# Kernel tuning notes

Hardware: AMD Instinct MI355X
Metric: run time of the kernel (lower is better)

## Reference

```python
import jax, jax.numpy as jnp
import numpy as np

N_NODES = 100000
N_EDGES = 1600000
IN_FEATS = 256
OUT_FEATS = 128


def setup_inputs() -> dict:
    key = jax.random.key(0)
    k1, k2, k3, k4, k5 = jax.random.split(key, 5)
    x = jax.random.normal(k1, (N_NODES, IN_FEATS), dtype=jnp.float32)
    edge_row = jax.random.randint(k2, (N_EDGES,), 0, N_NODES, dtype=jnp.int64 if jax.config.jax_enable_x64 else jnp.int32)
    edge_col = jax.random.randint(k3, (N_EDGES,), 0, N_NODES, dtype=jnp.int64 if jax.config.jax_enable_x64 else jnp.int32)
    edge_val = jax.random.uniform(k4, (N_EDGES,), dtype=jnp.float32)
    # xavier_uniform-like init for weight
    limit = float(np.sqrt(6.0 / (IN_FEATS + OUT_FEATS)))
    weight = jax.random.uniform(k5, (IN_FEATS, OUT_FEATS), dtype=jnp.float32, minval=-limit, maxval=limit)
    b = jnp.zeros((OUT_FEATS,), dtype=jnp.float32)
    return {"x": x, "edge_row": edge_row, "edge_col": edge_col, "edge_val": edge_val, "weight": weight, "b": b}


def reference(x, edge_row, edge_col, edge_val, weight, b):
    # sup = input @ weight : [N, out_feats]
    sup = x @ weight
    # out = spmm(adj, sup): gather source rows, scale by edge value, scatter-add to dest
    msgs = edge_val[:, None] * sup[edge_col]          # [E, out_feats]
    out = jax.ops.segment_sum(msgs, edge_row, num_segments=N_NODES)  # [N, out_feats]
    return out + b
```

## Files before the change

### kernel.cpp

```cpp
#include <hip/hip_runtime.h>


#define K_FEATS 256
#define N_FEATS 128
#define BSHIFT 7
#define BROWS 128
#define BCAP 3072
#define STASH 12
#define CHUNK 8192
#define EPT 32
#define RMOD 5

typedef __attribute__((ext_vector_type(8))) short short8;
typedef __attribute__((ext_vector_type(4))) float float4v;

__device__ __forceinline__ unsigned short f2bf(float f) {
    unsigned int u = __float_as_uint(f);
    unsigned int r = u + 0x7FFF + ((u >> 16) & 1);
    return (unsigned short)(r >> 16);
}

__global__ __launch_bounds__(256) void prep_w(const float* __restrict__ w,
                                              unsigned short* __restrict__ wt) {
    int n = blockIdx.x;
    int k = threadIdx.x;
    wt[n * K_FEATS + k] = f2bf(w[k * N_FEATS + n]);
}

__global__ __launch_bounds__(256) void zero_ints(int* __restrict__ p, int n) {
    int i = blockIdx.x * 256 + threadIdx.x;
    if (i < n) p[i] = 0;
}

__global__ __launch_bounds__(256) void gemm_partition(
        const float* __restrict__ x, const unsigned short* __restrict__ wt,
        unsigned short* __restrict__ sup, int M, int NT,
        const int* __restrict__ erow, const int* __restrict__ ecol,
        const float* __restrict__ eval_, int* __restrict__ bcur,
        int2* __restrict__ tmp, int E, int NB, int NCH) {
    __shared__ int hist[1024];
    __shared__ int cur[1024];
    const int g   = blockIdx.x;
    const int tid = threadIdx.x;

    if (g % RMOD == 0) {
        int pid = g / RMOD;
        if (pid >= NCH) return;
        const long e0 = (long)pid * CHUNK;

        for (int i = tid; i < NB; i += 256) hist[i] = 0;
        __syncthreads();

        int rows[EPT];
#pragma unroll
        for (int i = 0; i < EPT; i++) {
            long e = e0 + tid + i * 256;
            int r = -1;
            if (e < E) {
                r = erow[e];
                atomicAdd(&hist[r >> BSHIFT], 1);
            }
            rows[i] = r;
        }
        __syncthreads();

        for (int i = tid; i < NB; i += 256) {
            int c = hist[i];
            cur[i] = c ? atomicAdd(&bcur[i], c) : 0;
        }
        __syncthreads();

#pragma unroll
        for (int i = 0; i < EPT; i++) {
            long e = e0 + tid + i * 256;
            if (e >= E) continue;
            int r = rows[i];
            int b = r >> BSHIFT;
            int p = atomicAdd(&cur[b], 1);
            if (p < BCAP)
                tmp[(long)b * BCAP + p] = make_int2(((r & (BROWS - 1)) << 17) | ecol[e],
                                                    __float_as_int(eval_[e]));
        }
        return;
    }

    int tile = g - g / RMOD - 1;
    if (tile >= NT) return;

    const int wv   = tid >> 6;
    const int lane = tid & 63;
    const int l15  = lane & 15;
    const int quad = lane >> 4;
    const int row0 = tile * 128 + wv * 32;

    float4v acc[2][8];
#pragma unroll
    for (int mt = 0; mt < 2; mt++)
#pragma unroll
        for (int nt = 0; nt < 8; nt++) acc[mt][nt] = (float4v)(0.f);

#pragma unroll 2
    for (int k0 = 0; k0 < K_FEATS; k0 += 32) {
        short8 afrag[2];
#pragma unroll
        for (int mt = 0; mt < 2; mt++) {
            int grow = row0 + mt * 16 + l15;
            float4 a0 = make_float4(0.f, 0.f, 0.f, 0.f);
            float4 a1 = make_float4(0.f, 0.f, 0.f, 0.f);
            if (grow < M) {
                const float* p = x + (long)grow * K_FEATS + k0 + quad * 8;
                a0 = *(const float4*)p;
                a1 = *(const float4*)(p + 4);
            }
            short8 af;
            af[0] = (short)f2bf(a0.x); af[1] = (short)f2bf(a0.y);
            af[2] = (short)f2bf(a0.z); af[3] = (short)f2bf(a0.w);
            af[4] = (short)f2bf(a1.x); af[5] = (short)f2bf(a1.y);
            af[6] = (short)f2bf(a1.z); af[7] = (short)f2bf(a1.w);
            afrag[mt] = af;
        }
        short8 bfrag[8];
#pragma unroll
        for (int nt = 0; nt < 8; nt++) {
            bfrag[nt] = *(const short8*)(wt + (nt * 16 + l15) * K_FEATS + k0 + quad * 8);
        }
#pragma unroll
        for (int mt = 0; mt < 2; mt++)
#pragma unroll
            for (int nt = 0; nt < 8; nt++)
                acc[mt][nt] = __builtin_amdgcn_mfma_f32_16x16x32_bf16(
                    afrag[mt], bfrag[nt], acc[mt][nt], 0, 0, 0);
    }

#pragma unroll
    for (int mt = 0; mt < 2; mt++) {
#pragma unroll
        for (int reg = 0; reg < 4; reg++) {
            int grow = row0 + mt * 16 + quad * 4 + reg;
            if (grow < M) {
#pragma unroll
                for (int nt = 0; nt < 8; nt++) {
                    sup[(long)grow * N_FEATS + nt * 16 + l15] = f2bf(acc[mt][nt][reg]);
                }
            }
        }
    }
}

__global__ __launch_bounds__(256) void bucket_spmm(const int* __restrict__ bcnt,
                                                   const int2* __restrict__ tmp,
                                                   const unsigned short* __restrict__ sup,
                                                   const float* __restrict__ b,
                                                   float* __restrict__ out, int M) {
    __shared__ int hist[BROWS];
    __shared__ int rs[BROWS];
    __shared__ int cur[BROWS];
    __shared__ __align__(16) int2 se[BCAP];
    const int bkt  = blockIdx.x;
    const int tid  = threadIdx.x;
    const int wv   = tid >> 6;
    const int lane = tid & 63;
    const int row0 = bkt << BSHIFT;

    if (tid < BROWS) hist[tid] = 0;
    __syncthreads();

    int cnt = bcnt[bkt];
    if (cnt > BCAP) cnt = BCAP;
    const int2* t = tmp + (long)bkt * BCAP;

    int2 stash[STASH];
#pragma unroll
    for (int j = 0; j < STASH; j++) {
        int i = tid + j * 256;
        if (i < cnt) {
            int2 e = t[i];
            stash[j] = e;
            atomicAdd(&hist[(unsigned)e.x >> 17], 1);
        }
    }
    __syncthreads();

    if (tid < BROWS) cur[tid] = hist[tid];
    __syncthreads();
#pragma unroll
    for (int s = 1; s < BROWS; s <<= 1) {
        int v = 0;
        if (tid >= s && tid < BROWS) v = cur[tid - s];
        __syncthreads();
        if (tid < BROWS) cur[tid] += v;
        __syncthreads();
    }
    if (tid < BROWS) {
        int start = cur[tid] - hist[tid];
        rs[tid]  = start;
        cur[tid] = start;
    }
    __syncthreads();

#pragma unroll
    for (int j = 0; j < STASH; j++) {
        int i = tid + j * 256;
        if (i < cnt) {
            int2 e = stash[j];
            int rl = (unsigned)e.x >> 17;
            int p = atomicAdd(&cur[rl], 1);
            se[p] = make_int2(e.x & 0x1FFFF, e.y);
        }
    }
    __syncthreads();

    const int half = lane >> 5;
    const int l31  = lane & 31;
    const uint2* sup64 = (const uint2*)sup;
    const float4v bb = ((const float4v*)b)[l31];

    for (int rr = 0; rr < 32; rr++) {
        int r    = wv * 32 + rr;
        int grow = row0 + r;
        if (grow >= M) break;
        int s  = rs[r];
        int e2 = s + hist[r];

        float4v acc = (float4v)(0.f);
        int base = s;
        for (; base + 8 <= e2; base += 8) {
            int2 ed[4];
#pragma unroll
            for (int u = 0; u < 4; u++) ed[u] = se[base + half + 2 * u];
            uint2 g[4];
#pragma unroll
            for (int u = 0; u < 4; u++) g[u] = sup64[(long)ed[u].x * 32 + l31];
#pragma unroll
            for (int u = 0; u < 4; u++) {
                float v = __int_as_float(ed[u].y);
                acc.x += v * __uint_as_float(g[u].x << 16);
                acc.y += v * __uint_as_float(g[u].x & 0xFFFF0000u);
                acc.z += v * __uint_as_float(g[u].y << 16);
                acc.w += v * __uint_as_float(g[u].y & 0xFFFF0000u);
            }
        }
        for (int i = base + half; i < e2; i += 2) {
            int2 ed = se[i];
            uint2 g = sup64[(long)ed.x * 32 + l31];
            float v = __int_as_float(ed.y);
            acc.x += v * __uint_as_float(g.x << 16);
            acc.y += v * __uint_as_float(g.x & 0xFFFF0000u);
            acc.z += v * __uint_as_float(g.y << 16);
            acc.w += v * __uint_as_float(g.y & 0xFFFF0000u);
        }

        acc.x += __shfl_xor(acc.x, 32);
        acc.y += __shfl_xor(acc.y, 32);
        acc.z += __shfl_xor(acc.z, 32);
        acc.w += __shfl_xor(acc.w, 32);

        if (half == 0) {
            float4v o = acc + bb;
            *(float4v*)(out + (long)grow * N_FEATS + l31 * 4) = o;
        }
    }
}

extern "C" void kernel_launch(void* const* d_in, const int* in_sizes, int n_in,
                              void* d_out, int out_size, void* d_ws, size_t ws_size,
                              hipStream_t stream) {
    const float* x     = (const float*)d_in[0];
    const int*   erow  = (const int*)d_in[1];
    const int*   ecol  = (const int*)d_in[2];
    const float* eval_ = (const float*)d_in[3];
    const float* w     = (const float*)d_in[4];
    const float* b     = (const float*)d_in[5];
    float* out = (float*)d_out;

    const int M   = in_sizes[0] / K_FEATS;
    const int E   = in_sizes[1];
    const int NB  = (M + BROWS - 1) >> BSHIFT;
    const int NT  = (M + 127) / 128;
    const int NCH = (E + CHUNK - 1) / CHUNK;

    size_t o_sup  = 0;
    size_t o_wt   = o_sup  + (((size_t)M * N_FEATS * 2 + 15) & ~15ul);
    size_t o_bcur = o_wt   + (size_t)K_FEATS * N_FEATS * 2;
    size_t o_tmp  = o_bcur + (((size_t)NB * 4 + 15) & ~15ul);

    unsigned short* sup  = (unsigned short*)((char*)d_ws + o_sup);
    unsigned short* wt   = (unsigned short*)((char*)d_ws + o_wt);
    int*            bcur = (int*)((char*)d_ws + o_bcur);
    int2*           tmp  = (int2*)((char*)d_ws + o_tmp);

    prep_w<<<N_FEATS, 256, 0, stream>>>(w, wt);
    zero_ints<<<(NB + 255) / 256, 256, 0, stream>>>(bcur, NB);

    gemm_partition<<<NT + NCH, 256, 0, stream>>>(x, wt, sup, M, NT,
                                                 erow, ecol, eval_, bcur, tmp, E, NB, NCH);

    bucket_spmm<<<NB, 256, 0, stream>>>(bcur, tmp, sup, b, out, M);
}
```

Baseline: 317.5 us.

## Split GEMM into bf16 conversion pass and LDS-staged MFMA GEMM; widen SpMM blocks

The fused partition kernel now only converts x to bf16 into a workspace buffer alongside the edge bucketing. A separate GEMM kernel streams the bf16 tiles into swizzled LDS with global_load_lds before the MFMA loop. The bucket SpMM runs 512-thread blocks with half the per-thread stash and 16 rows per wave. This trades an extra pass over x (fp32 read plus bf16 write and re-read) for cheaper, LDS-fed GEMM loads and more parallelism in the SpMM.

```diff
diff --git a/kernel.cpp b/kernel.cpp
--- a/kernel.cpp
+++ b/kernel.cpp
@@ -6,13 +6,16 @@
 #define BSHIFT 7
 #define BROWS 128
 #define BCAP 3072
-#define STASH 12
+#define STASH 6
 #define CHUNK 8192
 #define EPT 32
 #define RMOD 5
 
 typedef __attribute__((ext_vector_type(8))) short short8;
 typedef __attribute__((ext_vector_type(4))) float float4v;
+
+typedef const unsigned int __attribute__((address_space(1)))* gld_src_t;
+typedef unsigned int __attribute__((address_space(3)))* gld_dst_t;
 
 __device__ __forceinline__ unsigned short f2bf(float f) {
     unsigned int u = __float_as_uint(f);
@@ -32,9 +35,8 @@
     if (i < n) p[i] = 0;
 }
 
-__global__ __launch_bounds__(256) void gemm_partition(
-        const float* __restrict__ x, const unsigned short* __restrict__ wt,
-        unsigned short* __restrict__ sup, int M, int NT,
+__global__ __launch_bounds__(256) void conv_partition(
+        const float* __restrict__ x, unsigned short* __restrict__ xb, int M,
         const int* __restrict__ erow, const int* __restrict__ ecol,
         const float* __restrict__ eval_, int* __restrict__ bcur,
         int2* __restrict__ tmp, int E, int NB, int NCH) {
@@ -85,13 +87,37 @@
     }
 
     int tile = g - g / RMOD - 1;
-    if (tile >= NT) return;
-
+    const int row0 = tile * 128;
+#pragma unroll
+    for (int j = 0; j < 16; j++) {
+        long idx  = (long)row0 * K_FEATS + j * 2048 + tid * 8;
+        int  grow = row0 + j * 8 + (tid >> 5);
+        short8 o;
+        if (grow < M) {
+            float4 v0 = *(const float4*)(x + idx);
+            float4 v1 = *(const float4*)(x + idx + 4);
+            o[0] = (short)f2bf(v0.x); o[1] = (short)f2bf(v0.y);
+            o[2] = (short)f2bf(v0.z); o[3] = (short)f2bf(v0.w);
+            o[4] = (short)f2bf(v1.x); o[5] = (short)f2bf(v1.y);
+            o[6] = (short)f2bf(v1.z); o[7] = (short)f2bf(v1.w);
+        } else {
+            o = (short8)(short)0;
+        }
+        *(short8*)(xb + idx) = o;
+    }
+}
+
+__global__ __launch_bounds__(256) void gcn_gemm(const unsigned short* __restrict__ xb,
+                                                const unsigned short* __restrict__ wt,
+                                                unsigned short* __restrict__ sup, int M) {
+    __shared__ __align__(16) unsigned char As[16384];
+
+    const int tid  = threadIdx.x;
     const int wv   = tid >> 6;
     const int lane = tid & 63;
     const int l15  = lane & 15;
     const int quad = lane >> 4;
-    const int row0 = tile * 128 + wv * 32;
+    const int row0 = blockIdx.x * 128;
 
     float4v acc[2][8];
 #pragma unroll
@@ -99,44 +125,51 @@
 #pragma unroll
         for (int nt = 0; nt < 8; nt++) acc[mt][nt] = (float4v)(0.f);
 
-#pragma unroll 2
-    for (int k0 = 0; k0 < K_FEATS; k0 += 32) {
-        short8 afrag[2];
-#pragma unroll
-        for (int mt = 0; mt < 2; mt++) {
-            int grow = row0 + mt * 16 + l15;
-            float4 a0 = make_float4(0.f, 0.f, 0.f, 0.f);
-            float4 a1 = make_float4(0.f, 0.f, 0.f, 0.f);
-            if (grow < M) {
-                const float* p = x + (long)grow * K_FEATS + k0 + quad * 8;
-                a0 = *(const float4*)p;
-                a1 = *(const float4*)(p + 4);
-            }
-            short8 af;
-            af[0] = (short)f2bf(a0.x); af[1] = (short)f2bf(a0.y);
-            af[2] = (short)f2bf(a0.z); af[3] = (short)f2bf(a0.w);
-            af[4] = (short)f2bf(a1.x); af[5] = (short)f2bf(a1.y);
-            af[6] = (short)f2bf(a1.z); af[7] = (short)f2bf(a1.w);
-            afrag[mt] = af;
-        }
-        short8 bfrag[8];
-#pragma unroll
-        for (int nt = 0; nt < 8; nt++) {
-            bfrag[nt] = *(const short8*)(wt + (nt * 16 + l15) * K_FEATS + k0 + quad * 8);
-        }
-#pragma unroll
-        for (int mt = 0; mt < 2; mt++)
-#pragma unroll
-            for (int nt = 0; nt < 8; nt++)
-                acc[mt][nt] = __builtin_amdgcn_mfma_f32_16x16x32_bf16(
-                    afrag[mt], bfrag[nt], acc[mt][nt], 0, 0, 0);
+    for (int ks = 0; ks < 4; ks++) {
+#pragma unroll
+        for (int i = 0; i < 4; i++) {
+            int s   = i * 4 + wv;
+            int off = (s << 10) + (lane << 4);
+            int row = off >> 7;
+            int cp  = off & 127;
+            int c   = cp ^ ((row & 7) << 4);
+            const char* src = (const char*)xb + (((long)(row0 + row)) << 9) + (ks << 7) + c;
+            __builtin_amdgcn_global_load_lds((gld_src_t)(const void*)src,
+                                             (gld_dst_t)(void*)(As + (s << 10)), 16, 0, 0);
+        }
+        __syncthreads();
+
+#pragma unroll
+        for (int subk = 0; subk < 2; subk++) {
+            const int k0 = ks * 64 + subk * 32;
+            short8 afrag[2];
+#pragma unroll
+            for (int mt = 0; mt < 2; mt++) {
+                int row  = wv * 32 + mt * 16 + l15;
+                int byte = (row << 7) + subk * 64 + quad * 16;
+                byte ^= (row & 7) << 4;
+                afrag[mt] = *(const short8*)(As + byte);
+            }
+            short8 bfrag[8];
+#pragma unroll
+            for (int nt = 0; nt < 8; nt++) {
+                bfrag[nt] = *(const short8*)(wt + (nt * 16 + l15) * K_FEATS + k0 + quad * 8);
+            }
+#pragma unroll
+            for (int mt = 0; mt < 2; mt++)
+#pragma unroll
+                for (int nt = 0; nt < 8; nt++)
+                    acc[mt][nt] = __builtin_amdgcn_mfma_f32_16x16x32_bf16(
+                        afrag[mt], bfrag[nt], acc[mt][nt], 0, 0, 0);
+        }
+        __syncthreads();
     }
 
 #pragma unroll
     for (int mt = 0; mt < 2; mt++) {
 #pragma unroll
         for (int reg = 0; reg < 4; reg++) {
-            int grow = row0 + mt * 16 + quad * 4 + reg;
+            int grow = row0 + wv * 32 + mt * 16 + quad * 4 + reg;
             if (grow < M) {
 #pragma unroll
                 for (int nt = 0; nt < 8; nt++) {
@@ -147,7 +180,7 @@
     }
 }
 
-__global__ __launch_bounds__(256) void bucket_spmm(const int* __restrict__ bcnt,
+__global__ __launch_bounds__(512) void bucket_spmm(const int* __restrict__ bcnt,
                                                    const int2* __restrict__ tmp,
                                                    const unsigned short* __restrict__ sup,
                                                    const float* __restrict__ b,
@@ -172,7 +205,7 @@
     int2 stash[STASH];
 #pragma unroll
     for (int j = 0; j < STASH; j++) {
-        int i = tid + j * 256;
+        int i = tid + j * 512;
         if (i < cnt) {
             int2 e = t[i];
             stash[j] = e;
@@ -200,7 +233,7 @@
 
 #pragma unroll
     for (int j = 0; j < STASH; j++) {
-        int i = tid + j * 256;
+        int i = tid + j * 512;
         if (i < cnt) {
             int2 e = stash[j];
             int rl = (unsigned)e.x >> 17;
@@ -215,8 +248,8 @@
     const uint2* sup64 = (const uint2*)sup;
     const float4v bb = ((const float4v*)b)[l31];
 
-    for (int rr = 0; rr < 32; rr++) {
-        int r    = wv * 32 + rr;
+    for (int rr = 0; rr < 16; rr++) {
+        int r    = wv * 16 + rr;
         int grow = row0 + r;
         if (grow >= M) break;
         int s  = rs[r];
@@ -280,11 +313,13 @@
     const int NCH = (E + CHUNK - 1) / CHUNK;
 
     size_t o_sup  = 0;
-    size_t o_wt   = o_sup  + (((size_t)M * N_FEATS * 2 + 15) & ~15ul);
+    size_t o_xb   = o_sup  + (((size_t)M * N_FEATS * 2 + 15) & ~15ul);
+    size_t o_wt   = o_xb   + ((size_t)NT * 128 * K_FEATS * 2);
     size_t o_bcur = o_wt   + (size_t)K_FEATS * N_FEATS * 2;
     size_t o_tmp  = o_bcur + (((size_t)NB * 4 + 15) & ~15ul);
 
     unsigned short* sup  = (unsigned short*)((char*)d_ws + o_sup);
+    unsigned short* xb   = (unsigned short*)((char*)d_ws + o_xb);
     unsigned short* wt   = (unsigned short*)((char*)d_ws + o_wt);
     int*            bcur = (int*)((char*)d_ws + o_bcur);
     int2*           tmp  = (int2*)((char*)d_ws + o_tmp);
@@ -292,8 +327,10 @@
     prep_w<<<N_FEATS, 256, 0, stream>>>(w, wt);
     zero_ints<<<(NB + 255) / 256, 256, 0, stream>>>(bcur, NB);
 
-    gemm_partition<<<NT + NCH, 256, 0, stream>>>(x, wt, sup, M, NT,
+    conv_partition<<<NT + NCH, 256, 0, stream>>>(x, xb, M,
                                                  erow, ecol, eval_, bcur, tmp, E, NB, NCH);
 
-    bucket_spmm<<<NB, 256, 0, stream>>>(bcur, tmp, sup, b, out, M);
-}
+    gcn_gemm<<<NT, 256, 0, stream>>>(xb, wt, sup, M);
+
+    bucket_spmm<<<NB, 512, 0, stream>>>(bcur, tmp, sup, b, out, M);
+}
```

Result: slower. 332.3 us (+4.6%).
